# Kernel tuning notes

Hardware: AMD Instinct MI355X
Metric: run time of the kernel (lower is better)

Reference implementation:

```python
import jax, jax.numpy as jnp
import numpy as np

N = 100000   # nodes
E = 800000   # edges
F_IN = 256   # num_features
H = 256      # hidden_dim
C = 2        # num_classes
G = 128      # graphs in batch


def setup_inputs() -> dict:
    key = jax.random.key(0)
    ks = jax.random.split(key, 6)
    x = jax.random.normal(ks[0], (N, F_IN), jnp.float32)
    edge_index = jax.random.randint(ks[1], (2, E), 0, N, dtype=jnp.int64)
    # sorted graph ids, every one of the G graphs non-empty (global_max_pool needs no empty segments)
    batch = (jnp.arange(N, dtype=jnp.int64) * G) // N
    init = lambda k, shp, fan: jax.random.normal(k, shp, jnp.float32) / np.float32(np.sqrt(fan))
    W1 = init(ks[2], (F_IN, H), F_IN); b1 = jnp.zeros((H,), jnp.float32)
    W2 = init(ks[3], (H, H), H);       b2 = jnp.zeros((H,), jnp.float32)
    Wc = init(ks[4], (H, C), H);       bc = jnp.zeros((C,), jnp.float32)
    return dict(x=x, edge_index=edge_index, batch=batch,
                W1=W1, b1=b1, W2=W2, b2=b2, Wc=Wc, bc=bc)


def gcn_conv(x, W, b, row, col, n):
    """PyG GCNConv: h = D^-1/2 (A+I) D^-1/2 x W + b (row/col already include self-loops)."""
    h = x @ W                                                        # [n, out]
    deg = jax.ops.segment_sum(jnp.ones(col.shape, jnp.float32), col, num_segments=n)
    dinv = jnp.where(deg > 0, jax.lax.rsqrt(jnp.maximum(deg, 1.0)), 0.0)
    norm = dinv[row] * dinv[col]                                     # [E+n]
    out = jax.ops.segment_sum(h[row] * norm[:, None], col, num_segments=n)
    return out + b


def reference(x, edge_index, batch, W1, b1, W2, b2, Wc, bc):
    n = x.shape[0]
    loop = jnp.arange(n, dtype=edge_index.dtype)
    row = jnp.concatenate([edge_index[0], loop])   # add self-loops
    col = jnp.concatenate([edge_index[1], loop])
    h = jax.nn.relu(gcn_conv(x, W1, b1, row, col, n))
    # F.dropout(p=0.5) is identity in eval mode
    h = gcn_conv(h, W2, b2, row, col, n)
    g = jax.ops.segment_max(h, batch, num_segments=G)  # global_max_pool -> [G, H]
    logits = g @ Wc + bc
    return jax.nn.log_softmax(logits, axis=1)
```

## Files before the change

### kernel.cpp

```cpp
#include <hip/hip_runtime.h>
#include <hip/hip_bf16.h>

#define N_NODES 100000
#define N_EDGES 800000
#define HD 256
#define NG 128

__device__ __forceinline__ unsigned f2key(float f){
  unsigned u = __float_as_uint(f);
  return (u & 0x80000000u) ? ~u : (u | 0x80000000u);
}
__device__ __forceinline__ float key2f(unsigned k){
  unsigned u = (k & 0x80000000u) ? (k & 0x7FFFFFFFu) : ~k;
  return __uint_as_float(u);
}

__global__ void k_deg(const int* __restrict__ ei, int* __restrict__ deg){
  int e = blockIdx.x*256 + threadIdx.x;
  const int M = N_EDGES + N_NODES;
  if(e < M){
    int c = (e < N_EDGES) ? ei[N_EDGES + e] : (e - N_EDGES);
    atomicAdd(&deg[c], 1);
  }
}

__global__ void k_scan1(const int* __restrict__ deg, int* __restrict__ ptr,
                        int* __restrict__ partials){
  __shared__ int s[256];
  int tid = threadIdx.x;
  int i = blockIdx.x*256 + tid;
  int v = (i < N_NODES) ? deg[i] : 0;
  s[tid] = v; __syncthreads();
  for(int off=1; off<256; off<<=1){
    int t = (tid >= off) ? s[tid-off] : 0;
    __syncthreads();
    s[tid] += t;
    __syncthreads();
  }
  if(i < N_NODES) ptr[i] = s[tid] - v;
  if(tid == 255) partials[blockIdx.x] = s[255];
}

__global__ void k_scan2(int* __restrict__ partials, int nb, int* __restrict__ ptrN){
  if(threadIdx.x == 0 && blockIdx.x == 0){
    int run = 0;
    for(int b=0;b<nb;b++){ int t = partials[b]; partials[b] = run; run += t; }
    *ptrN = run;
  }
}

__global__ void k_scan3(int* __restrict__ ptr, const int* __restrict__ partials,
                        int* __restrict__ cursor){
  int i = blockIdx.x*256 + threadIdx.x;
  if(i < N_NODES){
    int v = ptr[i] + partials[blockIdx.x];
    ptr[i] = v; cursor[i] = v;
  }
}

__global__ void k_fill(const int* __restrict__ ei, int* __restrict__ cursor,
                       int* __restrict__ src){
  int e = blockIdx.x*256 + threadIdx.x;
  const int M = N_EDGES + N_NODES;
  if(e < M){
    int r, c;
    if(e < N_EDGES){ r = ei[e]; c = ei[N_EDGES + e]; }
    else           { r = c = e - N_EDGES; }
    int pos = atomicAdd(&cursor[c], 1);
    src[pos] = r;
  }
}

__global__ void k_dinv(const int* __restrict__ deg, float* __restrict__ dinv){
  int i = blockIdx.x*256 + threadIdx.x;
  if(i < N_NODES) dinv[i] = rsqrtf((float)deg[i]);
}

__global__ __launch_bounds__(256) void k_gemm(const float* __restrict__ A,
                                              const float* __restrict__ W,
                                              float* __restrict__ out){
  __shared__ float As[16][132];
  __shared__ float Bs[16][132];
  int tid = threadIdx.x;
  int ty = tid >> 4, tx = tid & 15;
  float acc[8][8];
  #pragma unroll
  for(int i=0;i<8;i++)
    #pragma unroll
    for(int j=0;j<8;j++) acc[i][j] = 0.f;

  int ar = tid >> 1;
  int ac = (tid & 1) << 3;
  int grow = blockIdx.x*128 + ar;
  int brow = tid >> 4;
  int bcol = (tid & 15) << 3;
  const float* aptr = A + (size_t)grow*HD + ac;
  const float* bptr = W + (size_t)brow*HD + blockIdx.y*128 + bcol;
  bool aval = grow < N_NODES;

  for(int k0=0;k0<HD;k0+=16){
    float4 a0 = make_float4(0,0,0,0), a1 = a0;
    if(aval){ a0 = *(const float4*)(aptr); a1 = *(const float4*)(aptr+4); }
    float4 b0 = *(const float4*)(bptr);
    float4 b1 = *(const float4*)(bptr+4);
    aptr += 16; bptr += (size_t)16*HD;
    __syncthreads();
    As[ac+0][ar]=a0.x; As[ac+1][ar]=a0.y; As[ac+2][ar]=a0.z; As[ac+3][ar]=a0.w;
    As[ac+4][ar]=a1.x; As[ac+5][ar]=a1.y; As[ac+6][ar]=a1.z; As[ac+7][ar]=a1.w;
    *(float4*)&Bs[brow][bcol]   = b0;
    *(float4*)&Bs[brow][bcol+4] = b1;
    __syncthreads();
    #pragma unroll
    for(int kk=0;kk<16;kk++){
      float a[8], b[8];
      *(float4*)&a[0] = *(const float4*)&As[kk][ty*8];
      *(float4*)&a[4] = *(const float4*)&As[kk][ty*8+4];
      *(float4*)&b[0] = *(const float4*)&Bs[kk][tx*8];
      *(float4*)&b[4] = *(const float4*)&Bs[kk][tx*8+4];
      #pragma unroll
      for(int i=0;i<8;i++)
        #pragma unroll
        for(int j=0;j<8;j++) acc[i][j] = fmaf(a[i], b[j], acc[i][j]);
    }
  }
  int rowBase = blockIdx.x*128 + ty*8;
  int colBase = blockIdx.y*128 + tx*8;
  #pragma unroll
  for(int i=0;i<8;i++){
    int r = rowBase + i;
    if(r < N_NODES){
      float4 v0 = make_float4(acc[i][0],acc[i][1],acc[i][2],acc[i][3]);
      float4 v1 = make_float4(acc[i][4],acc[i][5],acc[i][6],acc[i][7]);
      *(float4*)(out + (size_t)r*HD + colBase)     = v0;
      *(float4*)(out + (size_t)r*HD + colBase + 4) = v1;
    }
  }
}

template<int RELU, int POOL>
__global__ __launch_bounds__(256) void k_agg(const float* __restrict__ t,
    const int* __restrict__ ptr, const int* __restrict__ src,
    const float* __restrict__ dinv, const float* __restrict__ bias,
    float* __restrict__ out, unsigned* __restrict__ gkeys,
    const int* __restrict__ batch){
  int v = blockIdx.x*4 + (threadIdx.x >> 6);
  if(v >= N_NODES) return;
  int f = (threadIdx.x & 63) * 4;
  float4 acc = make_float4(0,0,0,0);
  int j0 = ptr[v], j1 = ptr[v+1];
  for(int j=j0;j<j1;j++){
    int r = src[j];
    float w = dinv[r];
    float4 hv = *(const float4*)(t + (size_t)r*HD + f);
    acc.x = fmaf(w, hv.x, acc.x);
    acc.y = fmaf(w, hv.y, acc.y);
    acc.z = fmaf(w, hv.z, acc.z);
    acc.w = fmaf(w, hv.w, acc.w);
  }
  float dv = dinv[v];
  float4 b4 = *(const float4*)(bias + f);
  acc.x = fmaf(acc.x, dv, b4.x);
  acc.y = fmaf(acc.y, dv, b4.y);
  acc.z = fmaf(acc.z, dv, b4.z);
  acc.w = fmaf(acc.w, dv, b4.w);
  if(RELU){
    acc.x = fmaxf(acc.x, 0.f); acc.y = fmaxf(acc.y, 0.f);
    acc.z = fmaxf(acc.z, 0.f); acc.w = fmaxf(acc.w, 0.f);
  }
  if(POOL){
    int g = batch[v];
    unsigned* gp = gkeys + (size_t)g*HD + f;
    atomicMax(gp+0, f2key(acc.x));
    atomicMax(gp+1, f2key(acc.y));
    atomicMax(gp+2, f2key(acc.z));
    atomicMax(gp+3, f2key(acc.w));
  } else {
    *(float4*)(out + (size_t)v*HD + f) = acc;
  }
}

__global__ void k_head(const unsigned* __restrict__ gk, const float* __restrict__ Wc,
                       const float* __restrict__ bc, float* __restrict__ out){
  int i = threadIdx.x;
  if(i >= NG) return;
  float a0 = 0.f, a1 = 0.f;
  for(int k=0;k<HD;k++){
    float gv = key2f(gk[(size_t)i*HD + k]);
    a0 = fmaf(gv, Wc[2*k],   a0);
    a1 = fmaf(gv, Wc[2*k+1], a1);
  }
  a0 += bc[0]; a1 += bc[1];
  float m = fmaxf(a0, a1);
  float lse = m + logf(expf(a0-m) + expf(a1-m));
  out[2*i]   = a0 - lse;
  out[2*i+1] = a1 - lse;
}

extern "C" void kernel_launch(void* const* d_in, const int* in_sizes, int n_in,
                              void* d_out, int out_size, void* d_ws, size_t ws_size,
                              hipStream_t stream){
  (void)in_sizes; (void)n_in; (void)out_size; (void)ws_size;
  const float* x   = (const float*)d_in[0];
  const int*   ei  = (const int*)d_in[1];
  const int*   bat = (const int*)d_in[2];
  const float* W1  = (const float*)d_in[3];
  const float* b1  = (const float*)d_in[4];
  const float* W2  = (const float*)d_in[5];
  const float* b2  = (const float*)d_in[6];
  const float* Wc  = (const float*)d_in[7];
  const float* bc  = (const float*)d_in[8];
  float* out = (float*)d_out;

  char* ws = (char*)d_ws;
  size_t off = 0;
  auto alloc = [&](size_t bytes)->void*{
    void* p = ws + off; off = (off + bytes + 255) & ~(size_t)255; return p;
  };
  float*    T      = (float*)alloc((size_t)N_NODES*HD*4);
  float*    Hb     = (float*)alloc((size_t)N_NODES*HD*4);
  int*      deg    = (int*)alloc((size_t)N_NODES*4);
  float*    dinv   = (float*)alloc((size_t)N_NODES*4);
  int*      ptr    = (int*)alloc((size_t)(N_NODES+1)*4);
  int*      cursor = (int*)alloc((size_t)N_NODES*4);
  int*      src    = (int*)alloc((size_t)(N_EDGES+N_NODES)*4);
  int*      partials = (int*)alloc(512*4);
  unsigned* gkeys  = (unsigned*)alloc((size_t)NG*HD*4);

  const int M = N_EDGES + N_NODES;
  const int nbM = (M + 255)/256;
  const int nbN = (N_NODES + 255)/256;

  hipMemsetAsync(deg,   0, (size_t)N_NODES*4, stream);
  hipMemsetAsync(gkeys, 0, (size_t)NG*HD*4,   stream);

  k_deg  <<<nbM, 256, 0, stream>>>(ei, deg);
  k_scan1<<<nbN, 256, 0, stream>>>(deg, ptr, partials);
  k_scan2<<<1,   64,  0, stream>>>(partials, nbN, ptr + N_NODES);
  k_scan3<<<nbN, 256, 0, stream>>>(ptr, partials, cursor);
  k_fill <<<nbM, 256, 0, stream>>>(ei, cursor, src);
  k_dinv <<<nbN, 256, 0, stream>>>(deg, dinv);

  dim3 ggrid((N_NODES + 127)/128, HD/128);
  k_gemm<<<ggrid, 256, 0, stream>>>(x, W1, T);
  k_agg<1,0><<<(N_NODES+3)/4, 256, 0, stream>>>(T, ptr, src, dinv, b1, Hb, nullptr, nullptr);
  k_gemm<<<ggrid, 256, 0, stream>>>(Hb, W2, T);
  k_agg<0,1><<<(N_NODES+3)/4, 256, 0, stream>>>(T, ptr, src, dinv, b2, nullptr, gkeys, bat);
  k_head<<<1, 128, 0, stream>>>(gkeys, Wc, bc, out);
}
```

Measured before the change: 1.275 ms.

## Fold source-degree scaling into GEMM epilogue and unroll aggregation gathers by eight

The GEMM epilogue now multiplies each output row by dinv of that node, so the aggregation no longer loads dinv[src] per edge and becomes a plain sum. The aggregation loop is unrolled by eight, issuing all index loads and then all row gathers together so more memory requests are in flight. A masked tail handles leftover edges by gathering a valid row and multiplying it by a zero weight. The cost is higher register use and some redundant loads in the tail.

```diff
diff --git a/kernel.cpp b/kernel.cpp
--- a/kernel.cpp
+++ b/kernel.cpp
@@ -78,6 +78,7 @@
 
 __global__ __launch_bounds__(256) void k_gemm(const float* __restrict__ A,
                                               const float* __restrict__ W,
+                                              const float* __restrict__ scale,
                                               float* __restrict__ out){
   __shared__ float As[16][132];
   __shared__ float Bs[16][132];
@@ -129,8 +130,9 @@
   for(int i=0;i<8;i++){
     int r = rowBase + i;
     if(r < N_NODES){
-      float4 v0 = make_float4(acc[i][0],acc[i][1],acc[i][2],acc[i][3]);
-      float4 v1 = make_float4(acc[i][4],acc[i][5],acc[i][6],acc[i][7]);
+      float s = scale[r];
+      float4 v0 = make_float4(acc[i][0]*s,acc[i][1]*s,acc[i][2]*s,acc[i][3]*s);
+      float4 v1 = make_float4(acc[i][4]*s,acc[i][5]*s,acc[i][6]*s,acc[i][7]*s);
       *(float4*)(out + (size_t)r*HD + colBase)     = v0;
       *(float4*)(out + (size_t)r*HD + colBase + 4) = v1;
     }
@@ -146,23 +148,48 @@
   int v = blockIdx.x*4 + (threadIdx.x >> 6);
   if(v >= N_NODES) return;
   int f = (threadIdx.x & 63) * 4;
-  float4 acc = make_float4(0,0,0,0);
+  float ax=0.f, ay=0.f, az=0.f, aw=0.f;
   int j0 = ptr[v], j1 = ptr[v+1];
-  for(int j=j0;j<j1;j++){
-    int r = src[j];
-    float w = dinv[r];
-    float4 hv = *(const float4*)(t + (size_t)r*HD + f);
-    acc.x = fmaf(w, hv.x, acc.x);
-    acc.y = fmaf(w, hv.y, acc.y);
-    acc.z = fmaf(w, hv.z, acc.z);
-    acc.w = fmaf(w, hv.w, acc.w);
-  }
+
+  int j = j0;
+  for(; j + 8 <= j1; j += 8){
+    int idx[8];
+    #pragma unroll
+    for(int u=0;u<8;u++) idx[u] = src[j+u];
+    float4 h[8];
+    #pragma unroll
+    for(int u=0;u<8;u++) h[u] = *(const float4*)(t + (size_t)idx[u]*HD + f);
+    #pragma unroll
+    for(int u=0;u<8;u++){
+      ax += h[u].x; ay += h[u].y; az += h[u].z; aw += h[u].w;
+    }
+  }
+  if(j < j1){
+    int idx[8]; float w[8];
+    #pragma unroll
+    for(int u=0;u<8;u++){
+      int jj = j+u;
+      bool act = jj < j1;
+      idx[u] = act ? src[jj] : src[j0];
+      w[u] = act ? 1.f : 0.f;
+    }
+    float4 h[8];
+    #pragma unroll
+    for(int u=0;u<8;u++) h[u] = *(const float4*)(t + (size_t)idx[u]*HD + f);
+    #pragma unroll
+    for(int u=0;u<8;u++){
+      ax = fmaf(w[u], h[u].x, ax); ay = fmaf(w[u], h[u].y, ay);
+      az = fmaf(w[u], h[u].z, az); aw = fmaf(w[u], h[u].w, aw);
+    }
+  }
+
   float dv = dinv[v];
   float4 b4 = *(const float4*)(bias + f);
-  acc.x = fmaf(acc.x, dv, b4.x);
-  acc.y = fmaf(acc.y, dv, b4.y);
-  acc.z = fmaf(acc.z, dv, b4.z);
-  acc.w = fmaf(acc.w, dv, b4.w);
+  float4 acc;
+  acc.x = fmaf(ax, dv, b4.x);
+  acc.y = fmaf(ay, dv, b4.y);
+  acc.z = fmaf(az, dv, b4.z);
+  acc.w = fmaf(aw, dv, b4.w);
   if(RELU){
     acc.x = fmaxf(acc.x, 0.f); acc.y = fmaxf(acc.y, 0.f);
     acc.z = fmaxf(acc.z, 0.f); acc.w = fmaxf(acc.w, 0.f);
@@ -241,9 +268,9 @@
   k_dinv <<<nbN, 256, 0, stream>>>(deg, dinv);
 
   dim3 ggrid((N_NODES + 127)/128, HD/128);
-  k_gemm<<<ggrid, 256, 0, stream>>>(x, W1, T);
+  k_gemm<<<ggrid, 256, 0, stream>>>(x, W1, dinv, T);
   k_agg<1,0><<<(N_NODES+3)/4, 256, 0, stream>>>(T, ptr, src, dinv, b1, Hb, nullptr, nullptr);
-  k_gemm<<<ggrid, 256, 0, stream>>>(Hb, W2, T);
+  k_gemm<<<ggrid, 256, 0, stream>>>(Hb, W2, dinv, T);
   k_agg<0,1><<<(N_NODES+3)/4, 256, 0, stream>>>(T, ptr, src, dinv, b2, nullptr, gkeys, bat);
   k_head<<<1, 128, 0, stream>>>(gkeys, Wc, bc, out);
 }
```

After: 1.267 ms. Within noise of the previous version (-0.7%).

## Prescale GEMM rows by dinv and batch 8 neighbor gathers per aggregation step

Applied to the files above, without the earlier changes.

The GEMM epilogue now multiplies each output row by dinv[r], so the aggregation kernel no longer gathers dinv for every neighbor. The aggregation loop issues eight independent inline-asm global loads per iteration with clamped indices and 0/1 masks, then waits once. This is meant to raise memory-level parallelism on the irregular gathers and remove the per-edge dependent dinv load. In exchange, the tail iterations issue redundant loads, and the inline asm with vmcnt(0) limits what the compiler can schedule.

```diff
diff --git a/kernel.cpp b/kernel.cpp
--- a/kernel.cpp
+++ b/kernel.cpp
@@ -78,6 +78,7 @@
 
 __global__ __launch_bounds__(256) void k_gemm(const float* __restrict__ A,
                                               const float* __restrict__ W,
+                                              const float* __restrict__ scale,
                                               float* __restrict__ out){
   __shared__ float As[16][132];
   __shared__ float Bs[16][132];
@@ -129,8 +130,9 @@
   for(int i=0;i<8;i++){
     int r = rowBase + i;
     if(r < N_NODES){
-      float4 v0 = make_float4(acc[i][0],acc[i][1],acc[i][2],acc[i][3]);
-      float4 v1 = make_float4(acc[i][4],acc[i][5],acc[i][6],acc[i][7]);
+      float s = scale[r];
+      float4 v0 = make_float4(acc[i][0]*s,acc[i][1]*s,acc[i][2]*s,acc[i][3]*s);
+      float4 v1 = make_float4(acc[i][4]*s,acc[i][5]*s,acc[i][6]*s,acc[i][7]*s);
       *(float4*)(out + (size_t)r*HD + colBase)     = v0;
       *(float4*)(out + (size_t)r*HD + colBase + 4) = v1;
     }
@@ -145,31 +147,78 @@
     const int* __restrict__ batch){
   int v = blockIdx.x*4 + (threadIdx.x >> 6);
   if(v >= N_NODES) return;
-  int f = (threadIdx.x & 63) * 4;
-  float4 acc = make_float4(0,0,0,0);
+  const int lane = threadIdx.x & 63;
+  const float* tl = t + lane*4;
+
   int j0 = ptr[v], j1 = ptr[v+1];
-  for(int j=j0;j<j1;j++){
-    int r = src[j];
-    float w = dinv[r];
-    float4 hv = *(const float4*)(t + (size_t)r*HD + f);
-    acc.x = fmaf(w, hv.x, acc.x);
-    acc.y = fmaf(w, hv.y, acc.y);
-    acc.z = fmaf(w, hv.z, acc.z);
-    acc.w = fmaf(w, hv.w, acc.w);
-  }
   float dv = dinv[v];
+  int gidx = 0;
+  if(POOL) gidx = batch[v];
+  const int last = j1 - 1;
+
+  float a0=0.f, a1=0.f, a2=0.f, a3=0.f;
+
+  for(int j=j0; j<j1; j+=8){
+    int jc1=j+1>last?last:j+1, jc2=j+2>last?last:j+2, jc3=j+3>last?last:j+3;
+    int jc4=j+4>last?last:j+4, jc5=j+5>last?last:j+5, jc6=j+6>last?last:j+6;
+    int jc7=j+7>last?last:j+7;
+    int i0=src[j],   i1=src[jc1], i2=src[jc2], i3=src[jc3];
+    int i4=src[jc4], i5=src[jc5], i6=src[jc6], i7=src[jc7];
+    float w1=(j+1<j1)?1.f:0.f, w2=(j+2<j1)?1.f:0.f, w3=(j+3<j1)?1.f:0.f;
+    float w4=(j+4<j1)?1.f:0.f, w5=(j+5<j1)?1.f:0.f, w6=(j+6<j1)?1.f:0.f;
+    float w7=(j+7<j1)?1.f:0.f;
+
+    const float* p0 = tl + (size_t)i0*HD;
+    const float* p1 = tl + (size_t)i1*HD;
+    const float* p2 = tl + (size_t)i2*HD;
+    const float* p3 = tl + (size_t)i3*HD;
+    const float* p4 = tl + (size_t)i4*HD;
+    const float* p5 = tl + (size_t)i5*HD;
+    const float* p6 = tl + (size_t)i6*HD;
+    const float* p7 = tl + (size_t)i7*HD;
+
+    float4 d0,d1,d2,d3,d4,d5,d6,d7;
+    asm volatile("global_load_dwordx4 %0, %1, off" : "=v"(d0) : "v"(p0));
+    asm volatile("global_load_dwordx4 %0, %1, off" : "=v"(d1) : "v"(p1));
+    asm volatile("global_load_dwordx4 %0, %1, off" : "=v"(d2) : "v"(p2));
+    asm volatile("global_load_dwordx4 %0, %1, off" : "=v"(d3) : "v"(p3));
+    asm volatile("global_load_dwordx4 %0, %1, off" : "=v"(d4) : "v"(p4));
+    asm volatile("global_load_dwordx4 %0, %1, off" : "=v"(d5) : "v"(p5));
+    asm volatile("global_load_dwordx4 %0, %1, off" : "=v"(d6) : "v"(p6));
+    asm volatile("global_load_dwordx4 %0, %1, off" : "=v"(d7) : "v"(p7));
+    asm volatile("s_waitcnt vmcnt(0)" ::: "memory");
+    __builtin_amdgcn_sched_barrier(0);
+
+    a0 += d0.x; a1 += d0.y; a2 += d0.z; a3 += d0.w;
+    a0 = fmaf(w1, d1.x, a0); a1 = fmaf(w1, d1.y, a1);
+    a2 = fmaf(w1, d1.z, a2); a3 = fmaf(w1, d1.w, a3);
+    a0 = fmaf(w2, d2.x, a0); a1 = fmaf(w2, d2.y, a1);
+    a2 = fmaf(w2, d2.z, a2); a3 = fmaf(w2, d2.w, a3);
+    a0 = fmaf(w3, d3.x, a0); a1 = fmaf(w3, d3.y, a1);
+    a2 = fmaf(w3, d3.z, a2); a3 = fmaf(w3, d3.w, a3);
+    a0 = fmaf(w4, d4.x, a0); a1 = fmaf(w4, d4.y, a1);
+    a2 = fmaf(w4, d4.z, a2); a3 = fmaf(w4, d4.w, a3);
+    a0 = fmaf(w5, d5.x, a0); a1 = fmaf(w5, d5.y, a1);
+    a2 = fmaf(w5, d5.z, a2); a3 = fmaf(w5, d5.w, a3);
+    a0 = fmaf(w6, d6.x, a0); a1 = fmaf(w6, d6.y, a1);
+    a2 = fmaf(w6, d6.z, a2); a3 = fmaf(w6, d6.w, a3);
+    a0 = fmaf(w7, d7.x, a0); a1 = fmaf(w7, d7.y, a1);
+    a2 = fmaf(w7, d7.z, a2); a3 = fmaf(w7, d7.w, a3);
+  }
+
+  int f = lane*4;
   float4 b4 = *(const float4*)(bias + f);
-  acc.x = fmaf(acc.x, dv, b4.x);
-  acc.y = fmaf(acc.y, dv, b4.y);
-  acc.z = fmaf(acc.z, dv, b4.z);
-  acc.w = fmaf(acc.w, dv, b4.w);
+  float4 acc;
+  acc.x = fmaf(a0, dv, b4.x);
+  acc.y = fmaf(a1, dv, b4.y);
+  acc.z = fmaf(a2, dv, b4.z);
+  acc.w = fmaf(a3, dv, b4.w);
   if(RELU){
     acc.x = fmaxf(acc.x, 0.f); acc.y = fmaxf(acc.y, 0.f);
     acc.z = fmaxf(acc.z, 0.f); acc.w = fmaxf(acc.w, 0.f);
   }
   if(POOL){
-    int g = batch[v];
-    unsigned* gp = gkeys + (size_t)g*HD + f;
+    unsigned* gp = gkeys + (size_t)gidx*HD + f;
     atomicMax(gp+0, f2key(acc.x));
     atomicMax(gp+1, f2key(acc.y));
     atomicMax(gp+2, f2key(acc.z));
@@ -241,9 +290,9 @@
   k_dinv <<<nbN, 256, 0, stream>>>(deg, dinv);
 
   dim3 ggrid((N_NODES + 127)/128, HD/128);
-  k_gemm<<<ggrid, 256, 0, stream>>>(x, W1, T);
+  k_gemm<<<ggrid, 256, 0, stream>>>(x, W1, dinv, T);
   k_agg<1,0><<<(N_NODES+3)/4, 256, 0, stream>>>(T, ptr, src, dinv, b1, Hb, nullptr, nullptr);
-  k_gemm<<<ggrid, 256, 0, stream>>>(Hb, W2, T);
+  k_gemm<<<ggrid, 256, 0, stream>>>(Hb, W2, dinv, T);
   k_agg<0,1><<<(N_NODES+3)/4, 256, 0, stream>>>(T, ptr, src, dinv, b2, nullptr, gkeys, bat);
   k_head<<<1, 128, 0, stream>>>(gkeys, Wc, bc, out);
 }
```

After: 1.262 ms. About the same (-1.0%).
